# Kernel optimization log

Measured on AMD Instinct MI355X. Metric: run time of the kernel, lower is better.

Reference implementation:

```python
import jax, jax.numpy as jnp
import numpy as np

D_MODEL = 1024
N_HEADS = 16
DH = D_MODEL // N_HEADS
ROPE_THETA = 10000.0


def rotate_half(u):
    h = u.shape[-1] // 2
    return jnp.concatenate([-u[..., h:], u[..., :h]], axis=-1)


def apply_rope(q, k, cos, sin):
    return q * cos + rotate_half(q) * sin, k * cos + rotate_half(k) * sin


def setup_inputs() -> dict:
    key = jax.random.key(0)
    ks = jax.random.split(key, 6)
    B, S = 2, 2048
    x = jax.random.normal(ks[0], (B, S, D_MODEL), dtype=jnp.float32)
    y = jax.random.normal(ks[1], (B, S, D_MODEL), dtype=jnp.float32)
    wq = 0.01 * jax.random.normal(ks[2], (D_MODEL, D_MODEL), dtype=jnp.float32)
    wk = 0.01 * jax.random.normal(ks[3], (D_MODEL, D_MODEL), dtype=jnp.float32)
    wv = 0.01 * jax.random.normal(ks[4], (D_MODEL, D_MODEL), dtype=jnp.float32)
    wo = 0.01 * jax.random.normal(ks[5], (D_MODEL, D_MODEL), dtype=jnp.float32)
    return {"x": x, "y": y, "wq": wq, "wk": wk, "wv": wv, "wo": wo}


def reference(x, y, wq, wk, wv, wo):
    B, S, D = x.shape
    past_length = 0  # default; kv_cache=None

    Q = x @ wq.T                      # (B,S,D)
    K = y                             # NOTE: K is y un-projected (as in source)
    V = y @ wv.T
    # K1 = x @ wk.T is computed in the source but immediately overwritten
    # by the buggy second apply_rope call -> wk is unused in the output.
    V1 = x @ wo.T

    def heads(t):
        return t.reshape(B, S, N_HEADS, DH).transpose(0, 2, 1, 3)  # (B,H,S,dh)

    q_h, k_h, v_h, v1_h = heads(Q), heads(K), heads(V), heads(V1)

    # RoPE tables (past_length:past_length+S rows of the cache)
    freqs = 1.0 / ROPE_THETA ** (jnp.arange(0, DH, 2, dtype=jnp.float32) / DH)
    emb = jnp.arange(past_length, past_length + S, dtype=jnp.float32)[:, None] * freqs[None, :]
    cos = jnp.concatenate([jnp.cos(emb), jnp.cos(emb)], axis=-1)[None, None]  # (1,1,S,dh)
    sin = jnp.concatenate([jnp.sin(emb), jnp.sin(emb)], axis=-1)[None, None]

    q_h, k_h = apply_rope(q_h, k_h, cos, sin)
    # faithful to source: k1 = rope applied AGAIN to the already-roped k
    _, k1_h = apply_rope(q_h, k_h, cos, sin)

    k_full = jnp.concatenate([k_h, k1_h], axis=2)   # (B,H,2S,dh)
    v_full = jnp.concatenate([v_h, v1_h], axis=2)
    S_full = k_full.shape[2]

    # mask: tril(diagonal=past_length) over (S,S_full), last S cols = eye(S)
    rows = jnp.arange(S)[:, None]
    cols = jnp.arange(S_full)[None, :]
    mask = cols <= rows + past_length
    mask = mask.at[:, -S:].set(jnp.eye(S, dtype=bool))  # (S,S_full)

    scores = jnp.einsum("bhqd,bhkd->bhqk", q_h, k_full) / jnp.sqrt(jnp.asarray(DH, x.dtype))
    scores = jnp.where(mask[None, None], scores, jnp.asarray(-1e30, x.dtype))
    attn = jax.nn.softmax(scores, axis=-1)
    out = jnp.einsum("bhqk,bhkd->bhqd", attn, v_full)
    out = out.transpose(0, 2, 1, 3).reshape(B, S, D)

    k_ret = k_full[:, :, :-S, :]
    return out, k_ret
```

## Files before the change

### kernel.cpp

```cpp
#include <hip/hip_runtime.h>

#define DM 1024
#define NHEADS 16
#define DHEAD 64
#define BB 2
#define SS 2048
#define BH (BB*NHEADS)

typedef __attribute__((ext_vector_type(8))) short short8;
typedef __attribute__((ext_vector_type(4))) float float4v;
typedef unsigned short ushort_t;

#define LN1E4_D32 0.28782313662425572f

static __device__ __forceinline__ unsigned short f2bf(float f) {
    union { float f; unsigned u; } v; v.f = f;
    unsigned r = v.u + 0x7fffu + ((v.u >> 16) & 1u);
    return (unsigned short)(r >> 16);
}
static __device__ __forceinline__ float bf2f(unsigned short u) {
    union { float f; unsigned u; } v; v.u = ((unsigned)u) << 16;
    return v.f;
}
static __device__ __forceinline__ unsigned cvtpk_bf16(float lo, float hi) {
    unsigned r;
    asm("v_cvt_pk_bf16_f32 %0, %1, %2" : "=v"(r) : "v"(lo), "v"(hi));
    return r;
}

static __device__ __forceinline__ void gload16(const ushort_t* g, ushort_t* l) {
    __builtin_amdgcn_global_load_lds(
        (const __attribute__((address_space(1))) void*)g,
        (__attribute__((address_space(3))) void*)l, 16, 0, 0);
}

__global__ __launch_bounds__(256) void cvt_tile_kernel(
        const float* __restrict__ x, const float* __restrict__ wq,
        const float* __restrict__ wv, const float* __restrict__ wo,
        ushort_t* __restrict__ xb, ushort_t* __restrict__ wqb,
        ushort_t* __restrict__ wvb, ushort_t* __restrict__ wob) {
    int C = blockIdx.x * 256 + threadIdx.x;
    int c  = C & 511;
    int tl = C >> 9;
    int rb = tl >> 5, kb = tl & 31;
    const float* src; ushort_t* dst; int r0;
    if (rb < 32)      { src = x;  r0 = rb * 128;        dst = xb  + (size_t)tl * 4096; }
    else if (rb < 40) { src = wq; r0 = (rb - 32) * 128; dst = wqb + (size_t)(((rb - 32) * 32) + kb) * 4096; }
    else if (rb < 48) { src = wv; r0 = (rb - 40) * 128; dst = wvb + (size_t)(((rb - 40) * 32) + kb) * 4096; }
    else              { src = wo; r0 = (rb - 48) * 128; dst = wob + (size_t)(((rb - 48) * 32) + kb) * 4096; }
    int row = c >> 2, g = c & 3;
    int kk3 = g ^ ((row >> 1) & 3);
    const float* s = src + (size_t)(r0 + row) * DM + kb * 32 + kk3 * 8;
    float4 a0 = *reinterpret_cast<const float4*>(s);
    float4 a1 = *reinterpret_cast<const float4*>(s + 4);
    short8 v;
    v[0] = (short)f2bf(a0.x); v[1] = (short)f2bf(a0.y);
    v[2] = (short)f2bf(a0.z); v[3] = (short)f2bf(a0.w);
    v[4] = (short)f2bf(a1.x); v[5] = (short)f2bf(a1.y);
    v[6] = (short)f2bf(a1.z); v[7] = (short)f2bf(a1.w);
    *reinterpret_cast<short8*>(dst + c * 8) = v;
}

__global__ __launch_bounds__(256) void rope_k_kernel(const float* __restrict__ y,
        float* __restrict__ kout, ushort_t* __restrict__ khb, ushort_t* __restrict__ yb) {
    int t = blockIdx.x * blockDim.x + threadIdx.x;
    int i8 = t & 3;
    int s  = (t >> 2) & (SS - 1);
    int bh = t >> 13;
    int h = bh & (NHEADS - 1), b = bh >> 4;

    const float* yp = y + ((size_t)(b * SS + s)) * DM + h * DHEAD + i8 * 8;
    float4 a0 = *reinterpret_cast<const float4*>(yp);
    float4 a1 = *reinterpret_cast<const float4*>(yp + 4);
    float4 b0 = *reinterpret_cast<const float4*>(yp + 32);
    float4 b1 = *reinterpret_cast<const float4*>(yp + 36);
    float u0[8] = {a0.x, a0.y, a0.z, a0.w, a1.x, a1.y, a1.z, a1.w};
    float u1[8] = {b0.x, b0.y, b0.z, b0.w, b1.x, b1.y, b1.z, b1.w};
    float lo[8], hi[8];
#pragma unroll
    for (int j = 0; j < 8; j++) {
        int i = i8 * 8 + j;
        float freq = __expf(-(float)i * LN1E4_D32);
        float th = (float)s * freq;
        float cv = cosf(th), sv = sinf(th);
        lo[j] = u0[j] * cv - u1[j] * sv;
        hi[j] = u1[j] * cv + u0[j] * sv;
    }
    float* op = kout + ((size_t)bh * SS + s) * DHEAD + i8 * 8;
    *reinterpret_cast<float4*>(op)      = (float4){lo[0], lo[1], lo[2], lo[3]};
    *reinterpret_cast<float4*>(op + 4)  = (float4){lo[4], lo[5], lo[6], lo[7]};
    *reinterpret_cast<float4*>(op + 32) = (float4){hi[0], hi[1], hi[2], hi[3]};
    *reinterpret_cast<float4*>(op + 36) = (float4){hi[4], hi[5], hi[6], hi[7]};

    ushort_t* kb = khb + ((size_t)bh * 32 + (s >> 6)) * 4096 + (s & 63) * 64;
    short8 vlo, vhi;
#pragma unroll
    for (int j = 0; j < 8; j++) { vlo[j] = (short)f2bf(lo[j]); vhi[j] = (short)f2bf(hi[j]); }
    *reinterpret_cast<short8*>(kb + ((i8 ^ (s & 7)) << 3))       = vlo;
    *reinterpret_cast<short8*>(kb + (((i8 + 4) ^ (s & 7)) << 3)) = vhi;

    int rowm = b * SS + s;
    int rowin = rowm & 127, rbm = rowm >> 7;
    int g = i8 ^ ((rowin >> 1) & 3);
    ushort_t* yt = yb + ((size_t)(rbm * 32 + h * 2)) * 4096 + rowin * 32 + (g << 3);
    short8 ulo, uhi;
#pragma unroll
    for (int j = 0; j < 8; j++) { ulo[j] = (short)f2bf(u0[j]); uhi[j] = (short)f2bf(u1[j]); }
    *reinterpret_cast<short8*>(yt)        = ulo;
    *reinterpret_cast<short8*>(yt + 4096) = uhi;
}

__global__ __launch_bounds__(256, 2) void gemm3_kernel(
        const ushort_t* __restrict__ xb, const ushort_t* __restrict__ yb,
        const ushort_t* __restrict__ wqb, const ushort_t* __restrict__ wvb,
        const ushort_t* __restrict__ wob,
        ushort_t* __restrict__ qh, ushort_t* __restrict__ vt, ushort_t* __restrict__ v1h) {
    __shared__ __align__(16) char smem[34816];
    ushort_t* As = (ushort_t*)smem;
    ushort_t* Bs = (ushort_t*)(smem + 16384);
    ushort_t (*Ct)[136] = (ushort_t(*)[136])smem;

    int bid = blockIdx.x;
    int xcd = bid & 7;
    int s_  = bid >> 3;
    int zo  = s_ >> 5;
    int z   = (zo == 0) ? 0 : (zo == 1 ? 2 : 1);
    int t_  = s_ & 31;
    int n0  = (t_ >> 2) * 128;
    int m0  = (xcd * 4 + (t_ & 3)) * 128;

    const ushort_t* A = (z == 1) ? yb : xb;
    const ushort_t* W = (z == 0) ? wqb : (z == 1 ? wvb : wob);
    ushort_t* O = (z == 0) ? qh : (z == 1 ? vt : v1h);

    const ushort_t* Atl = A + (size_t)(m0 >> 7) * 32 * 4096;
    const ushort_t* Wtl = W + (size_t)(n0 >> 7) * 32 * 4096;

    int tid = threadIdx.x;
    int wave = tid >> 6, lane = tid & 63, quad = lane >> 4, l15 = lane & 15;
    int wr = (wave >> 1) * 64, wc = (wave & 1) * 64;

    int gi0 = tid * 8, gi1 = (256 + tid) * 8;
    int li0 = (tid & 192) * 8, li1 = (256 + (tid & 192)) * 8;

    int aoff[4], boff[4];
#pragma unroll
    for (int mi = 0; mi < 4; mi++) {
        int row = wr + mi * 16 + l15;
        aoff[mi] = row * 32 + ((quad ^ ((row >> 1) & 3)) << 3);
    }
#pragma unroll
    for (int ni = 0; ni < 4; ni++) {
        int row = wc + ni * 16 + l15;
        boff[ni] = row * 32 + ((quad ^ ((row >> 1) & 3)) << 3);
    }

    float4v acc[4][4];
#pragma unroll
    for (int a = 0; a < 4; a++)
#pragma unroll
        for (int b = 0; b < 4; b++)
            acc[a][b] = (float4v){0.f, 0.f, 0.f, 0.f};

    gload16(Atl + gi0, As + li0); gload16(Atl + gi1, As + li1);
    gload16(Wtl + gi0, Bs + li0); gload16(Wtl + gi1, Bs + li1);
    int cur = 0;

    for (int kb = 0; kb < 32; kb++) {
        __syncthreads();
        if (kb + 1 < 32) {
            const ushort_t* at = Atl + (size_t)(kb + 1) * 4096;
            const ushort_t* wt = Wtl + (size_t)(kb + 1) * 4096;
            int nb = (cur ^ 1) * 4096;
            gload16(at + gi0, As + nb + li0); gload16(at + gi1, As + nb + li1);
            gload16(wt + gi0, Bs + nb + li0); gload16(wt + gi1, Bs + nb + li1);
        }
        const ushort_t* Ac = As + cur * 4096;
        const ushort_t* Bc = Bs + cur * 4096;
        short8 af[4], bfr[4];
#pragma unroll
        for (int mi = 0; mi < 4; mi++)
            af[mi] = *reinterpret_cast<const short8*>(&Ac[aoff[mi]]);
#pragma unroll
        for (int ni = 0; ni < 4; ni++)
            bfr[ni] = *reinterpret_cast<const short8*>(&Bc[boff[ni]]);
#pragma unroll
        for (int mi = 0; mi < 4; mi++)
#pragma unroll
            for (int ni = 0; ni < 4; ni++)
                acc[mi][ni] = __builtin_amdgcn_mfma_f32_16x16x32_bf16(af[mi], bfr[ni], acc[mi][ni], 0, 0, 0);
        cur ^= 1;
    }

    if (z == 0) {
#pragma unroll
        for (int mi = 0; mi < 4; mi++)
#pragma unroll
            for (int r = 0; r < 4; r++) {
                int m = m0 + wr + mi * 16 + quad * 4 + r;
                float pos = (float)(m & (SS - 1));
#pragma unroll
                for (int ni = 0; ni < 2; ni++) {
                    int d = ni * 16 + l15;
                    float f = __expf(-(float)d * LN1E4_D32);
                    float th = pos * f;
                    float cv, sv;
                    __sincosf(th, &sv, &cv);
                    float u0 = acc[mi][ni][r], u1 = acc[mi][ni + 2][r];
                    acc[mi][ni][r]     = u0 * cv - u1 * sv;
                    acc[mi][ni + 2][r] = u1 * cv + u0 * sv;
                }
            }
    }

    __syncthreads();
#pragma unroll
    for (int mi = 0; mi < 4; mi++)
#pragma unroll
        for (int ni = 0; ni < 4; ni++) {
            int col = wc + ni * 16 + l15;
#pragma unroll
            for (int r = 0; r < 4; r++)
                Ct[wr + mi * 16 + quad * 4 + r][col] = f2bf(acc[mi][ni][r]);
        }
    __syncthreads();
    int h0 = n0 >> 6;
    if (z == 1) {
        int b = m0 >> 11;
        int s0 = m0 & (SS - 1);
#pragma unroll
        for (int it = 0; it < 8; it++) {
            int c = it * 256 + tid;
            int dh  = c & 63;
            int k16 = (c >> 6) & 15;
            int hh  = c >> 10;
            short8 v;
#pragma unroll
            for (int e = 0; e < 8; e++)
                v[e] = (short)Ct[k16 * 8 + e][hh * 64 + dh];
            int kt = (s0 >> 6) + (k16 >> 3);
            size_t off = ((size_t)((b * NHEADS + h0 + hh) * 32 + kt)) * 4096
                       + dh * 64 + (((k16 & 7) ^ (dh & 7)) << 3);
            *reinterpret_cast<short8*>(&O[off]) = v;
        }
    } else {
#pragma unroll
        for (int it = 0; it < 8; it++) {
            int c = it * 256 + tid;
            int o = c >> 3, j = c & 7;
            int hh = o >> 7, mr = o & 127;
            int m = m0 + mr, b = m >> 11, si = m & (SS - 1);
            uint4 v = *reinterpret_cast<const uint4*>(&Ct[mr][hh * 64 + j * 8]);
            *reinterpret_cast<uint4*>(
                &O[((size_t)((b * NHEADS + h0 + hh) * SS + si)) * DHEAD + j * 8]) = v;
        }
    }
}

template<bool MASKED>
static __device__ __forceinline__ void attn_tile(
        const ushort_t* __restrict__ Kc, const ushort_t* __restrict__ Vc, int kbase,
        int quad, int l15, int q0w, const short8* qf,
        ushort_t* __restrict__ Psw, float4v* Oa, float& lsum) {
    float4v sa[4];
#pragma unroll
    for (int t2 = 0; t2 < 4; t2++) sa[t2] = (float4v){0.f, 0.f, 0.f, 0.f};
#pragma unroll
    for (int t2 = 0; t2 < 4; t2++) {
        int key = t2 * 16 + l15;
        int ro = key * 64, sw = key & 7;
#pragma unroll
        for (int half = 0; half < 2; half++) {
            short8 kf = *reinterpret_cast<const short8*>(&Kc[ro + (((half * 4 + quad) ^ sw) << 3)]);
            sa[t2] = __builtin_amdgcn_mfma_f32_16x16x32_bf16(kf, qf[half], sa[t2], 0, 0, 0);
        }
    }
    int query = q0w + l15;
    int swl = l15 & 7;
#pragma unroll
    for (int t2 = 0; t2 < 4; t2++) {
        float p[4];
#pragma unroll
        for (int r = 0; r < 4; r++) {
            float e = __expf(sa[t2][r] * 0.125f);
            if (MASKED) {
                int key = kbase + t2 * 16 + quad * 4 + r;
                p[r] = (key <= query) ? e : 0.f;
            } else {
                p[r] = e;
            }
        }
        lsum += (p[0] + p[1]) + (p[2] + p[3]);
        unsigned w0 = cvtpk_bf16(p[0], p[1]);
        unsigned w1 = cvtpk_bf16(p[2], p[3]);
        int chunk = (((t2 * 2 + (quad >> 1)) ^ swl) << 3) + (quad & 1) * 4;
        *reinterpret_cast<unsigned*>(&Psw[l15 * 64 + chunk])     = w0;
        *reinterpret_cast<unsigned*>(&Psw[l15 * 64 + chunk + 2]) = w1;
    }
    short8 pf0 = *reinterpret_cast<const short8*>(&Psw[l15 * 64 + ((quad ^ swl) << 3)]);
    short8 pf1 = *reinterpret_cast<const short8*>(&Psw[l15 * 64 + (((4 + quad) ^ swl) << 3)]);
#pragma unroll
    for (int t = 0; t < 4; t++) {
        int dh = t * 16 + l15;
        int ro = dh * 64, sw = dh & 7;
        short8 vf0 = *reinterpret_cast<const short8*>(&Vc[ro + ((quad ^ sw) << 3)]);
        short8 vf1 = *reinterpret_cast<const short8*>(&Vc[ro + (((4 + quad) ^ sw) << 3)]);
        Oa[t] = __builtin_amdgcn_mfma_f32_16x16x32_bf16(pf0, vf0, Oa[t], 0, 0, 0);
        Oa[t] = __builtin_amdgcn_mfma_f32_16x16x32_bf16(pf1, vf1, Oa[t], 0, 0, 0);
    }
}

__global__ __launch_bounds__(512, 2) void attn_kernel(
        const ushort_t* __restrict__ qh, const float* __restrict__ kf32,
        const ushort_t* __restrict__ khb, const ushort_t* __restrict__ vtb,
        const ushort_t* __restrict__ v1h, float* __restrict__ out) {
    __shared__ __align__(16) ushort_t Ks[2][4096];
    __shared__ __align__(16) ushort_t Vt[2][4096];
    __shared__ __align__(16) ushort_t Ps[8][16][64];
    __shared__ float sdiag[8][16];
    __shared__ float sred[8][16];

    int bid = blockIdx.x;
    int bh = (bid & 7) * 4 + ((bid >> 3) & 3);
    int jq = 15 - (bid >> 5);
    int q0 = jq * 128;

    int tid = threadIdx.x, wave = tid >> 6, lane = tid & 63, quad = lane >> 4, l15 = lane & 15;
    int q0w = q0 + wave * 16;
    const ushort_t* qp  = qh  + (size_t)bh * SS * DHEAD;
    const float*    kp  = kf32 + (size_t)bh * SS * DHEAD;
    const ushort_t* v1p = v1h + (size_t)bh * SS * DHEAD;
    const ushort_t* ktb = khb + (size_t)bh * 32 * 4096;
    const ushort_t* vtt = vtb + (size_t)bh * 32 * 4096;

    short8 qf[2];
    qf[0] = *reinterpret_cast<const short8*>(&qp[(q0w + l15) * DHEAD + quad * 8]);
    qf[1] = *reinterpret_cast<const short8*>(&qp[(q0w + l15) * DHEAD + 32 + quad * 8]);

    float4v Oa[4];
#pragma unroll
    for (int t = 0; t < 4; t++) Oa[t] = (float4v){0.f, 0.f, 0.f, 0.f};
    float lsum = 0.f;

    int gi = tid * 8;
    int li = (tid & 448) * 8;

    int ntiles = jq * 2 + 2;
    gload16(ktb + gi, &Ks[0][li]);
    gload16(vtt + gi, &Vt[0][li]);
    int cur = 0;

    for (int kt = 0; kt < ntiles; kt++) {
        __syncthreads();
        if (kt + 1 < ntiles) {
            const ushort_t* gk = ktb + (size_t)(kt + 1) * 4096;
            const ushort_t* gv = vtt + (size_t)(kt + 1) * 4096;
            int nb = cur ^ 1;
            gload16(gk + gi, &Ks[nb][li]);
            gload16(gv + gi, &Vt[nb][li]);
        }
        int kbase = kt * 64;
        if (kbase <= q0w + 15) {
            if (kbase + 63 <= q0w)
                attn_tile<false>(Ks[cur], Vt[cur], kbase, quad, l15, q0w, qf,
                                 &Ps[wave][0][0], Oa, lsum);
            else
                attn_tile<true>(Ks[cur], Vt[cur], kbase, quad, l15, q0w, qf,
                                &Ps[wave][0][0], Oa, lsum);
        }
        cur ^= 1;
    }

    lsum += __shfl_xor(lsum, 16);
    lsum += __shfl_xor(lsum, 32);
    if (quad == 0) sred[wave][l15] = lsum;

    {
        int sk = q0w + l15;
        const float* krow = kp + (size_t)sk * DHEAD;
        short8 k1lo, k1hi;
#pragma unroll
        for (int j = 0; j < 8; j++) {
            int d = quad * 8 + j;
            float f = __expf(-(float)d * LN1E4_D32);
            float th = (float)sk * f;
            float cv, sv;
            __sincosf(th, &sv, &cv);
            float a = krow[d], b2 = krow[d + 32];
            k1lo[j] = (short)f2bf(a * cv - b2 * sv);
            k1hi[j] = (short)f2bf(b2 * cv + a * sv);
        }
        float4v sd4 = (float4v){0.f, 0.f, 0.f, 0.f};
        sd4 = __builtin_amdgcn_mfma_f32_16x16x32_bf16(qf[0], k1lo, sd4, 0, 0, 0);
        sd4 = __builtin_amdgcn_mfma_f32_16x16x32_bf16(qf[1], k1hi, sd4, 0, 0, 0);
#pragma unroll
        for (int r = 0; r < 4; r++)
            if (l15 == quad * 4 + r) sdiag[wave][l15] = sd4[r] * 0.125f;
        __syncthreads();

        int b = bh >> 4, h = bh & (NHEADS - 1);
#pragma unroll
        for (int r = 0; r < 4; r++) {
            float ls = sred[wave][quad * 4 + r];
            float pd = __expf(sdiag[wave][quad * 4 + r]);
            int query = q0w + quad * 4 + r;
            float linv = 1.f / (ls + pd);
#pragma unroll
            for (int t = 0; t < 4; t++) {
                float v1v = bf2f(v1p[query * DHEAD + t * 16 + l15]);
                float o = (Oa[t][r] + pd * v1v) * linv;
                out[(b * SS + query) * DM + h * DHEAD + t * 16 + l15] = o;
            }
        }
    }
}

extern "C" void kernel_launch(void* const* d_in, const int* in_sizes, int n_in,
                              void* d_out, int out_size, void* d_ws, size_t ws_size,
                              hipStream_t stream) {
    const float* x  = (const float*)d_in[0];
    const float* y  = (const float*)d_in[1];
    const float* wq = (const float*)d_in[2];
    const float* wv = (const float*)d_in[4];
    const float* wo = (const float*)d_in[5];
    float* outp  = (float*)d_out;
    float* k_out = outp + (size_t)BB * SS * DM;

    char* ws = (char*)d_ws;
    ushort_t* vtb = (ushort_t*)(ws);
    ushort_t* v1b = (ushort_t*)(ws + (8ull  << 20));
    ushort_t* qhb = (ushort_t*)(ws + (16ull << 20));
    ushort_t* khb = (ushort_t*)(ws + (24ull << 20));
    ushort_t* xb  = (ushort_t*)(ws + (32ull << 20));
    ushort_t* yb  = (ushort_t*)(ws + (40ull << 20));
    ushort_t* wqb = (ushort_t*)(ws + (48ull << 20));
    ushort_t* wvb = (ushort_t*)(ws + (50ull << 20));
    ushort_t* wob = (ushort_t*)(ws + (52ull << 20));

    cvt_tile_kernel<<<3584, 256, 0, stream>>>(x, wq, wv, wo, xb, wqb, wvb, wob);
    rope_k_kernel<<<1024, 256, 0, stream>>>(y, k_out, khb, yb);
    gemm3_kernel<<<768, 256, 0, stream>>>(xb, yb, wqb, wvb, wob, qhb, vtb, v1b);
    attn_kernel<<<512, 512, 0, stream>>>(qhb, k_out, khb, vtb, v1b, outp);
}
```

Baseline: 176.0 us.

## Merge prep kernels, shrink attention blocks to 64 queries, add MFMA priority hints

Combines the bf16 conversion kernel and the RoPE-K kernel into one launch, which removes one kernel boundary. Splits the attention grid into 1024 blocks of 4 waves covering 64 queries each, which cuts per-block K/V loading that is wasted on the causal triangle and improves load balance, at the cost of less K/V tile reuse per block. Wraps the MFMA sections in s_setprio to favour matrix issue. Shared scratch for the row sums and diagonal scores now reuses the per-wave P buffer.

```diff
diff --git a/kernel.cpp b/kernel.cpp
--- a/kernel.cpp
+++ b/kernel.cpp
@@ -34,36 +34,38 @@
         (__attribute__((address_space(3))) void*)l, 16, 0, 0);
 }
 
-__global__ __launch_bounds__(256) void cvt_tile_kernel(
-        const float* __restrict__ x, const float* __restrict__ wq,
-        const float* __restrict__ wv, const float* __restrict__ wo,
+__global__ __launch_bounds__(256) void prep_kernel(
+        const float* __restrict__ x, const float* __restrict__ y,
+        const float* __restrict__ wq, const float* __restrict__ wv,
+        const float* __restrict__ wo,
         ushort_t* __restrict__ xb, ushort_t* __restrict__ wqb,
-        ushort_t* __restrict__ wvb, ushort_t* __restrict__ wob) {
-    int C = blockIdx.x * 256 + threadIdx.x;
-    int c  = C & 511;
-    int tl = C >> 9;
-    int rb = tl >> 5, kb = tl & 31;
-    const float* src; ushort_t* dst; int r0;
-    if (rb < 32)      { src = x;  r0 = rb * 128;        dst = xb  + (size_t)tl * 4096; }
-    else if (rb < 40) { src = wq; r0 = (rb - 32) * 128; dst = wqb + (size_t)(((rb - 32) * 32) + kb) * 4096; }
-    else if (rb < 48) { src = wv; r0 = (rb - 40) * 128; dst = wvb + (size_t)(((rb - 40) * 32) + kb) * 4096; }
-    else              { src = wo; r0 = (rb - 48) * 128; dst = wob + (size_t)(((rb - 48) * 32) + kb) * 4096; }
-    int row = c >> 2, g = c & 3;
-    int kk3 = g ^ ((row >> 1) & 3);
-    const float* s = src + (size_t)(r0 + row) * DM + kb * 32 + kk3 * 8;
-    float4 a0 = *reinterpret_cast<const float4*>(s);
-    float4 a1 = *reinterpret_cast<const float4*>(s + 4);
-    short8 v;
-    v[0] = (short)f2bf(a0.x); v[1] = (short)f2bf(a0.y);
-    v[2] = (short)f2bf(a0.z); v[3] = (short)f2bf(a0.w);
-    v[4] = (short)f2bf(a1.x); v[5] = (short)f2bf(a1.y);
-    v[6] = (short)f2bf(a1.z); v[7] = (short)f2bf(a1.w);
-    *reinterpret_cast<short8*>(dst + c * 8) = v;
-}
-
-__global__ __launch_bounds__(256) void rope_k_kernel(const float* __restrict__ y,
-        float* __restrict__ kout, ushort_t* __restrict__ khb, ushort_t* __restrict__ yb) {
-    int t = blockIdx.x * blockDim.x + threadIdx.x;
+        ushort_t* __restrict__ wvb, ushort_t* __restrict__ wob,
+        float* __restrict__ kout, ushort_t* __restrict__ khb,
+        ushort_t* __restrict__ yb) {
+    if (blockIdx.x < 3584) {
+        int C = blockIdx.x * 256 + threadIdx.x;
+        int c  = C & 511;
+        int tl = C >> 9;
+        int rb = tl >> 5, kb = tl & 31;
+        const float* src; ushort_t* dst; int r0;
+        if (rb < 32)      { src = x;  r0 = rb * 128;        dst = xb  + (size_t)tl * 4096; }
+        else if (rb < 40) { src = wq; r0 = (rb - 32) * 128; dst = wqb + (size_t)(((rb - 32) * 32) + kb) * 4096; }
+        else if (rb < 48) { src = wv; r0 = (rb - 40) * 128; dst = wvb + (size_t)(((rb - 40) * 32) + kb) * 4096; }
+        else              { src = wo; r0 = (rb - 48) * 128; dst = wob + (size_t)(((rb - 48) * 32) + kb) * 4096; }
+        int row = c >> 2, g = c & 3;
+        int kk3 = g ^ ((row >> 1) & 3);
+        const float* s = src + (size_t)(r0 + row) * DM + kb * 32 + kk3 * 8;
+        float4 a0 = *reinterpret_cast<const float4*>(s);
+        float4 a1 = *reinterpret_cast<const float4*>(s + 4);
+        short8 v;
+        v[0] = (short)f2bf(a0.x); v[1] = (short)f2bf(a0.y);
+        v[2] = (short)f2bf(a0.z); v[3] = (short)f2bf(a0.w);
+        v[4] = (short)f2bf(a1.x); v[5] = (short)f2bf(a1.y);
+        v[6] = (short)f2bf(a1.z); v[7] = (short)f2bf(a1.w);
+        *reinterpret_cast<short8*>(dst + c * 8) = v;
+        return;
+    }
+    int t = (blockIdx.x - 3584) * 256 + threadIdx.x;
     int i8 = t & 3;
     int s  = (t >> 2) & (SS - 1);
     int bh = t >> 13;
@@ -265,6 +267,7 @@
     float4v sa[4];
 #pragma unroll
     for (int t2 = 0; t2 < 4; t2++) sa[t2] = (float4v){0.f, 0.f, 0.f, 0.f};
+    __builtin_amdgcn_s_setprio(1);
 #pragma unroll
     for (int t2 = 0; t2 < 4; t2++) {
         int key = t2 * 16 + l15;
@@ -275,6 +278,7 @@
             sa[t2] = __builtin_amdgcn_mfma_f32_16x16x32_bf16(kf, qf[half], sa[t2], 0, 0, 0);
         }
     }
+    __builtin_amdgcn_s_setprio(0);
     int query = q0w + l15;
     int swl = l15 & 7;
 #pragma unroll
@@ -299,6 +303,7 @@
     }
     short8 pf0 = *reinterpret_cast<const short8*>(&Psw[l15 * 64 + ((quad ^ swl) << 3)]);
     short8 pf1 = *reinterpret_cast<const short8*>(&Psw[l15 * 64 + (((4 + quad) ^ swl) << 3)]);
+    __builtin_amdgcn_s_setprio(1);
 #pragma unroll
     for (int t = 0; t < 4; t++) {
         int dh = t * 16 + l15;
@@ -308,22 +313,21 @@
         Oa[t] = __builtin_amdgcn_mfma_f32_16x16x32_bf16(pf0, vf0, Oa[t], 0, 0, 0);
         Oa[t] = __builtin_amdgcn_mfma_f32_16x16x32_bf16(pf1, vf1, Oa[t], 0, 0, 0);
     }
-}
-
-__global__ __launch_bounds__(512, 2) void attn_kernel(
+    __builtin_amdgcn_s_setprio(0);
+}
+
+__global__ __launch_bounds__(256, 4) void attn_kernel(
         const ushort_t* __restrict__ qh, const float* __restrict__ kf32,
         const ushort_t* __restrict__ khb, const ushort_t* __restrict__ vtb,
         const ushort_t* __restrict__ v1h, float* __restrict__ out) {
     __shared__ __align__(16) ushort_t Ks[2][4096];
     __shared__ __align__(16) ushort_t Vt[2][4096];
-    __shared__ __align__(16) ushort_t Ps[8][16][64];
-    __shared__ float sdiag[8][16];
-    __shared__ float sred[8][16];
+    __shared__ __align__(16) ushort_t Ps[4][1024];
 
     int bid = blockIdx.x;
     int bh = (bid & 7) * 4 + ((bid >> 3) & 3);
-    int jq = 15 - (bid >> 5);
-    int q0 = jq * 128;
+    int jq = 31 - (bid >> 5);
+    int q0 = jq * 64;
 
     int tid = threadIdx.x, wave = tid >> 6, lane = tid & 63, quad = lane >> 4, l15 = lane & 15;
     int q0w = q0 + wave * 16;
@@ -342,12 +346,12 @@
     for (int t = 0; t < 4; t++) Oa[t] = (float4v){0.f, 0.f, 0.f, 0.f};
     float lsum = 0.f;
 
-    int gi = tid * 8;
-    int li = (tid & 448) * 8;
-
-    int ntiles = jq * 2 + 2;
-    gload16(ktb + gi, &Ks[0][li]);
-    gload16(vtt + gi, &Vt[0][li]);
+    int gi0 = tid * 8, gi1 = (256 + tid) * 8;
+    int li0 = (tid & 192) * 8, li1 = (256 + (tid & 192)) * 8;
+
+    int ntiles = jq + 1;
+    gload16(ktb + gi0, &Ks[0][li0]); gload16(ktb + gi1, &Ks[0][li1]);
+    gload16(vtt + gi0, &Vt[0][li0]); gload16(vtt + gi1, &Vt[0][li1]);
     int cur = 0;
 
     for (int kt = 0; kt < ntiles; kt++) {
@@ -356,24 +360,27 @@
             const ushort_t* gk = ktb + (size_t)(kt + 1) * 4096;
             const ushort_t* gv = vtt + (size_t)(kt + 1) * 4096;
             int nb = cur ^ 1;
-            gload16(gk + gi, &Ks[nb][li]);
-            gload16(gv + gi, &Vt[nb][li]);
+            gload16(gk + gi0, &Ks[nb][li0]); gload16(gk + gi1, &Ks[nb][li1]);
+            gload16(gv + gi0, &Vt[nb][li0]); gload16(gv + gi1, &Vt[nb][li1]);
         }
         int kbase = kt * 64;
         if (kbase <= q0w + 15) {
             if (kbase + 63 <= q0w)
                 attn_tile<false>(Ks[cur], Vt[cur], kbase, quad, l15, q0w, qf,
-                                 &Ps[wave][0][0], Oa, lsum);
+                                 &Ps[wave][0], Oa, lsum);
             else
                 attn_tile<true>(Ks[cur], Vt[cur], kbase, quad, l15, q0w, qf,
-                                &Ps[wave][0][0], Oa, lsum);
+                                &Ps[wave][0], Oa, lsum);
         }
         cur ^= 1;
     }
+
+    float* sred  = reinterpret_cast<float*>(&Ps[wave][0]);
+    float* sdiag = reinterpret_cast<float*>(&Ps[wave][32]);
 
     lsum += __shfl_xor(lsum, 16);
     lsum += __shfl_xor(lsum, 32);
-    if (quad == 0) sred[wave][l15] = lsum;
+    if (quad == 0) sred[l15] = lsum;
 
     {
         int sk = q0w + l15;
@@ -395,14 +402,14 @@
         sd4 = __builtin_amdgcn_mfma_f32_16x16x32_bf16(qf[1], k1hi, sd4, 0, 0, 0);
 #pragma unroll
         for (int r = 0; r < 4; r++)
-            if (l15 == quad * 4 + r) sdiag[wave][l15] = sd4[r] * 0.125f;
+            if (l15 == quad * 4 + r) sdiag[l15] = sd4[r] * 0.125f;
         __syncthreads();
 
         int b = bh >> 4, h = bh & (NHEADS - 1);
 #pragma unroll
         for (int r = 0; r < 4; r++) {
-            float ls = sred[wave][quad * 4 + r];
-            float pd = __expf(sdiag[wave][quad * 4 + r]);
+            float ls = sred[quad * 4 + r];
+            float pd = __expf(sdiag[quad * 4 + r]);
             int query = q0w + quad * 4 + r;
             float linv = 1.f / (ls + pd);
 #pragma unroll
@@ -437,8 +444,8 @@
     ushort_t* wvb = (ushort_t*)(ws + (50ull << 20));
     ushort_t* wob = (ushort_t*)(ws + (52ull << 20));
 
-    cvt_tile_kernel<<<3584, 256, 0, stream>>>(x, wq, wv, wo, xb, wqb, wvb, wob);
-    rope_k_kernel<<<1024, 256, 0, stream>>>(y, k_out, khb, yb);
+    prep_kernel<<<4608, 256, 0, stream>>>(x, y, wq, wv, wo, xb, wqb, wvb, wob,
+                                          k_out, khb, yb);
     gemm3_kernel<<<768, 256, 0, stream>>>(xb, yb, wqb, wvb, wob, qhb, vtb, v1b);
-    attn_kernel<<<512, 512, 0, stream>>>(qhb, k_out, khb, vtb, v1b, outp);
-}
+    attn_kernel<<<1024, 256, 0, stream>>>(qhb, k_out, khb, vtb, v1b, outp);
+}
```

Result: no change. 173.2 us (-1.6%).
